# Kernel optimization log

Hardware: AMD Instinct MI355X
Metric: run time of the kernel (lower is better)

## Reference

```python
import jax, jax.numpy as jnp
import numpy as np
from jax import lax


def conv3d(x, w, b):
    # x: [B,C,H,W,D], w: [O,I,kh,kw,kd], SAME padding (matches padding=k//2 for odd k)
    out = lax.conv_general_dilated(
        x, w, window_strides=(1, 1, 1), padding='SAME',
        dimension_numbers=('NCDHW', 'OIDHW', 'NCDHW'))
    return out + b[None, :, None, None, None]


def setup_inputs() -> dict:
    key = jax.random.key(0)
    ks = jax.random.split(key, 9)
    B, C, H, W, D = 2, 64, 16, 16, 16
    P = 64  # pab_channels
    s = 0.05
    return {
        'x': jax.random.normal(ks[0], (B, C, H, W, D), jnp.float32),
        'top_w': jax.random.normal(ks[1], (P, C, 1, 1, 1), jnp.float32) * s,
        'top_b': jax.random.normal(ks[2], (P,), jnp.float32) * s,
        'center_w': jax.random.normal(ks[3], (P, C, 1, 1, 1), jnp.float32) * s,
        'center_b': jax.random.normal(ks[4], (P,), jnp.float32) * s,
        'bottom_w': jax.random.normal(ks[5], (C, C, 3, 3, 3), jnp.float32) * s,
        'bottom_b': jax.random.normal(ks[6], (C,), jnp.float32) * s,
        'out_w': jax.random.normal(ks[7], (C, C, 3, 3, 3), jnp.float32) * s,
        'out_b': jax.random.normal(ks[8], (C,), jnp.float32) * s,
    }


def reference(x, top_w, top_b, center_w, center_b, bottom_w, bottom_b, out_w, out_b):
    B, C, H, W, D = x.shape
    N = H * W * D
    x_top = conv3d(x, top_w, top_b).reshape(B, -1, N)            # [B,P,N]
    x_center = conv3d(x, center_w, center_b).reshape(B, -1, N)   # [B,P,N]
    x_bottom = conv3d(x, bottom_w, bottom_b).reshape(B, C, N)    # [B,C,N]
    # sp_map[b,n,m] = sum_p center[b,p,n] * top[b,p,m]
    sp = jnp.einsum('bpn,bpm->bnm', x_center, x_top)             # [B,N,N]
    # GLOBAL softmax over the entire flattened NxN map per batch element
    sp = jax.nn.softmax(sp.reshape(B, N * N), axis=1).reshape(B, N, N)
    sp = jnp.einsum('bnm,bcm->bnc', sp, x_bottom)                # [B,N,C]
    # faithful to torch: plain reshape [B,N,C] -> [B,C,H,W,D] (no transpose)
    sp = sp.reshape(B, C, H, W, D)
    return conv3d(x + sp, out_w, out_b)
```

## Files before the change

### kernel.cpp

```cpp
#include <hip/hip_runtime.h>


typedef __attribute__((ext_vector_type(8))) short bf16x8;
typedef __attribute__((ext_vector_type(4))) short short4v;
typedef __attribute__((ext_vector_type(4))) float f32x4;

#define DEVI static __device__ __forceinline__

DEVI f32x4 MFMA16(bf16x8 a, bf16x8 b, f32x4 c) {
  return __builtin_amdgcn_mfma_f32_16x16x32_bf16(a, b, c, 0, 0, 0);
}
DEVI f32x4 zero4() { return (f32x4){0.f, 0.f, 0.f, 0.f}; }

DEVI unsigned short f2bf(float f) {
  unsigned u = __float_as_uint(f);
  return (unsigned short)((u + 0x7fffu + ((u >> 16) & 1u)) >> 16);
}
DEVI float bf2f(unsigned short u) { return __uint_as_float((unsigned)u << 16); }
DEVI float fexp2(float x) { return __builtin_amdgcn_exp2f(x); }

DEVI void gll16(const unsigned short* g, unsigned short* l) {
  __builtin_amdgcn_global_load_lds(
      (const __attribute__((address_space(1))) void*)g,
      (__attribute__((address_space(3))) void*)l, 16, 0, 0);
}

__global__ void k_prep(const float* __restrict__ tw, const float* __restrict__ cw,
                       const float* __restrict__ bw, const float* __restrict__ ow,
                       const float* __restrict__ x,
                       unsigned short* __restrict__ wkTopF, unsigned short* __restrict__ wkCenF,
                       unsigned short* __restrict__ wkBotF, unsigned short* __restrict__ wkOutF,
                       unsigned short* __restrict__ xT, unsigned short* __restrict__ zbuf) {
  __shared__ float tile[64][65];
  int bx = blockIdx.x;
  int tid = threadIdx.x;
  if (bx == 0 && tid < 64) zbuf[tid] = 0;
  if (bx < 432) {
    int t = bx * 256 + tid;
    if (t < 4096) {
      int co = t >> 6, ci = t & 63;
      int cog = co >> 4, col = co & 15, kc = ci >> 5, kg = (ci & 31) >> 3, e = ci & 7;
      int dst = (((cog * 2 + kc) * 64) + col + 16 * kg) * 8 + e;
      wkTopF[dst] = f2bf(tw[t]);
      wkCenF[dst] = f2bf(cw[t]);
    }
    int k = t % 27;
    int ci = (t / 27) & 63;
    int co = t / (27 * 64);
    int cog = co >> 4, col = co & 15, kc = ci >> 5, kg = (ci & 31) >> 3, e = ci & 7;
    int dst = ((((cog * 27 + k) * 2 + kc) * 64) + col + 16 * kg) * 8 + e;
    wkBotF[dst] = f2bf(bw[t]);
    wkOutF[dst] = f2bf(ow[t]);
    return;
  }
  int bx2 = bx - 432;
  int b = bx2 >> 6;
  int n0 = (bx2 & 63) << 6;
  {
    int nl = tid & 63, cq = tid >> 6;
    const float* xb = x + (size_t)b * 262144;
#pragma unroll
    for (int j = 0; j < 16; j++) {
      int c = cq * 16 + j;
      tile[c][nl] = xb[(size_t)c * 4096 + n0 + nl];
    }
  }
  __syncthreads();
  {
    int n = tid >> 2, c0 = (tid & 3) << 4;
    bf16x8 o0, o1;
#pragma unroll
    for (int j = 0; j < 8; j++) {
      o0[j] = (short)f2bf(tile[c0 + j][n]);
      o1[j] = (short)f2bf(tile[c0 + 8 + j][n]);
    }
    unsigned short* dst = xT + ((size_t)(b * 4096 + n0 + n)) * 64 + c0;
    *(bf16x8*)(dst) = o0;
    *(bf16x8*)(dst + 8) = o1;
  }
}

template <int OMODE>
DEVI void conv3_body(int bx, int t,
                     const unsigned short* __restrict__ wkF,
                     const unsigned short* __restrict__ xTb,
                     const float* __restrict__ bias,
                     const unsigned short* __restrict__ zbuf,
                     float* __restrict__ outF, unsigned short* __restrict__ outH,
                     unsigned short* hl) {
  int ch = bx & 1, wp = (bx >> 1) & 7, h = (bx >> 4) & 15, b = bx >> 8;
  int lane = t & 63, w = t >> 6;
  int col = lane & 15, kg = lane >> 4;
  const unsigned short* xb = xTb + (size_t)b * 262144;
  int row8 = lane >> 3, blk = lane & 7;
#pragma unroll
  for (int q = 0; q < 6; q++) {
    int vi0 = w * 48 + q * 8;
    int vi = vi0 + row8;
    int dhv = vi >> 6, wv = (vi >> 4) & 3, dv = vi & 15;
    int hh = h + dhv - 1, ww = wp * 2 + wv - 1;
    bool val = ((unsigned)hh < 16u) & ((unsigned)ww < 16u);
    int sw = blk ^ (vi & 7);
    const unsigned short* src =
        val ? (xb + ((size_t)((hh * 256 + ww * 16 + dv)) << 6) + sw * 8) : (zbuf + blk * 8);
    gll16(src, hl + vi0 * 64);
  }
  __syncthreads();
  int wi = w >> 1;
  int cg = ch * 2 + (w & 1);
  const char* hlb = (const char*)hl;
  f32x4 acc0 = zero4(), acc1 = zero4();
#pragma unroll
  for (int k = 0; k < 27; k++) {
    const int dh = k / 9;
    const int dw = (k / 3) % 3;
    const int dz = k % 3 - 1;
    int dsum = col + dz;
    bool vd = (unsigned)dsum < 16u;
    int dcl = vd ? dsum : col;
    int sv = dh * 64 + (wi + dw) * 16 + dcl;
    const unsigned short* wfk = wkF + (((size_t)(cg * 27 + k)) << 10) + lane * 8;
#pragma unroll
    for (int kc = 0; kc < 2; kc++) {
      bf16x8 av = *(const bf16x8*)(wfk + (kc << 9));
      int g = (kc * 4 + kg) ^ (sv & 7);
      bf16x8 bv = *(const bf16x8*)(hlb + sv * 128 + g * 16);
      if (!vd) bv = (bf16x8){0, 0, 0, 0, 0, 0, 0, 0};
      if (kc == 0) acc0 = MFMA16(av, bv, acc0);
      else acc1 = MFMA16(av, bv, acc1);
    }
  }
  int n0c = h * 256 + (wp * 2 + wi) * 16 + col;
#pragma unroll
  for (int r = 0; r < 4; r++) {
    int co = ch * 32 + (w & 1) * 16 + kg * 4 + r;
    float v = acc0[r] + acc1[r] + bias[co];
    if (OMODE == 2)
      outH[(size_t)(b * 64 + co) * 4096 + n0c] = f2bf(v);
    else
      outF[(size_t)(b * 64 + co) * 4096 + n0c] = v;
  }
}

__global__ __launch_bounds__(256, 2) void k_convA(
    const unsigned short* __restrict__ wkTf, const unsigned short* __restrict__ wkCf,
    const unsigned short* __restrict__ wkBf, const unsigned short* __restrict__ xTb,
    const float* __restrict__ tbias, const float* __restrict__ cbias,
    const float* __restrict__ bbias, const unsigned short* __restrict__ zbuf,
    unsigned short* __restrict__ topT, unsigned short* __restrict__ cenT,
    unsigned short* __restrict__ botS) {
  __shared__ __align__(16) unsigned short hl[192 * 64];
  int bx0 = blockIdx.x;
  int t = threadIdx.x;
  if (bx0 >= 512) {
    conv3_body<2>(bx0 - 512, t, wkBf, xTb, bbias, zbuf, nullptr, botS, hl);
    return;
  }
  int lane = t & 63, wid = t >> 6;
  int col = lane & 15, kg = lane >> 4;
  int bx = bx0;
  int b = bx >> 8;
  int rest = bx & 255;
  int nt = rest >> 1, ch = rest & 1;
  int cg = ch * 2 + (wid >> 1);
  int co0 = ch * 32 + (wid >> 1) * 16;
  int n0c = nt * 32 + (wid & 1) * 16 + col;
  const unsigned short* xb = xTb + (size_t)b * 262144;
  f32x4 aT0 = zero4(), aT1 = zero4(), aC0 = zero4(), aC1 = zero4();
#pragma unroll
  for (int kc = 0; kc < 2; kc++) {
    bf16x8 bv = *(const bf16x8*)(xb + (size_t)n0c * 64 + kc * 32 + kg * 8);
    bf16x8 avT = *(const bf16x8*)(wkTf + (((size_t)cg * 2 + kc) * 64 + lane) * 8);
    bf16x8 avC = *(const bf16x8*)(wkCf + (((size_t)cg * 2 + kc) * 64 + lane) * 8);
    if (kc == 0) {
      aT0 = MFMA16(avT, bv, aT0);
      aC0 = MFMA16(avC, bv, aC0);
    } else {
      aT1 = MFMA16(avT, bv, aT1);
      aC1 = MFMA16(avC, bv, aC1);
    }
  }
  const float LOG2E = 1.4426950408889634f;
  short4v sT, sC;
#pragma unroll
  for (int r = 0; r < 4; r++) {
    float bvT = tbias[co0 + kg * 4 + r];
    float bvC = cbias[co0 + kg * 4 + r];
    sT[r] = (short)f2bf(aT0[r] + aT1[r] + bvT);
    sC[r] = (short)f2bf((aC0[r] + aC1[r] + bvC) * LOG2E);
  }
  size_t o = (size_t)(b * 4096 + n0c) * 64 + co0 + kg * 4;
  *(short4v*)(topT + o) = sT;
  *(short4v*)(cenT + o) = sC;
}

__global__ __launch_bounds__(256, 2) void k_convOut(
    const unsigned short* __restrict__ wkOf, const unsigned short* __restrict__ xTb,
    const float* __restrict__ bias, const unsigned short* __restrict__ zbuf,
    float* __restrict__ outF) {
  __shared__ __align__(16) unsigned short hl[192 * 64];
  conv3_body<1>(blockIdx.x, threadIdx.x, wkOf, xTb, bias, zbuf, outF, nullptr, hl);
}

__global__ __launch_bounds__(256, 2) void k_pass2(
    const unsigned short* __restrict__ cenT, const unsigned short* __restrict__ topT,
    const unsigned short* __restrict__ botS,
    unsigned short* __restrict__ part, float* __restrict__ Zpart) {
  __shared__ __align__(16) unsigned short topS[2][4096];
  __shared__ __align__(16) unsigned short botL[2][4096];
  __shared__ __align__(16) unsigned short pT[4][2][1024];
  __shared__ float zred[4];
  int bx = blockIdx.x;
  int b = bx >> 8;
  int ntp = (bx >> 3) & 31;
  int mc = bx & 7;
  int t = threadIdx.x;
  int lane = t & 63, w = t >> 6;
  int col = lane & 15, kg = lane >> 4;
  const unsigned short* cb = cenT + (size_t)b * 262144;
  const unsigned short* tb = topT + (size_t)b * 262144;
  const unsigned short* bb = botS + (size_t)b * 262144;
  int nA = ntp * 128 + w * 16;
  int mcBase = mc * 512;
  int row8 = lane >> 3, blk = lane & 7;
  int sw = blk ^ (row8 & 7);

  bf16x8 aA0 = *(const bf16x8*)(cb + (size_t)(nA + col) * 64 + kg * 8);
  bf16x8 aA1 = *(const bf16x8*)(cb + (size_t)(nA + col) * 64 + 32 + kg * 8);
  bf16x8 aB0 = *(const bf16x8*)(cb + (size_t)(nA + 64 + col) * 64 + kg * 8);
  bf16x8 aB1 = *(const bf16x8*)(cb + (size_t)(nA + 64 + col) * 64 + 32 + kg * 8);

  if (w < 2) {
#pragma unroll
    for (int q = 0; q < 4; q++) {
      int s = w * 4 + q;
      gll16(tb + (size_t)(mcBase + s * 8 + row8) * 64 + sw * 8, &topS[0][s * 512]);
    }
  } else {
#pragma unroll
    for (int q = 0; q < 4; q++) {
      int s = (w - 2) * 4 + q;
      gll16(bb + (size_t)(s * 8 + row8) * 4096 + mcBase + sw * 8, &botL[0][s * 512]);
    }
  }
  __syncthreads();

  f32x4 accOA[4], accOB[4];
#pragma unroll
  for (int ct = 0; ct < 4; ct++) {
    accOA[ct] = zero4();
    accOB[ct] = zero4();
  }
  float zs = 0.f;
  int swc = (col & 7) << 3;
  unsigned short* pw0 = &pT[w][0][0];
  unsigned short* pw1 = &pT[w][1][0];

  for (int j = 0; j < 8; j++) {
    int cur = j & 1;
    if (j < 7) {
      int m0n = mcBase + (j + 1) * 64;
      if (w < 2) {
#pragma unroll
        for (int q = 0; q < 4; q++) {
          int s = w * 4 + q;
          gll16(tb + (size_t)(m0n + s * 8 + row8) * 64 + sw * 8, &topS[cur ^ 1][s * 512]);
        }
      } else {
#pragma unroll
        for (int q = 0; q < 4; q++) {
          int s = (w - 2) * 4 + q;
          gll16(bb + (size_t)(s * 8 + row8) * 4096 + m0n + sw * 8, &botL[cur ^ 1][s * 512]);
        }
      }
    }
    f32x4 sA[4], sB[4];
#pragma unroll
    for (int mt = 0; mt < 4; mt++) {
      bf16x8 b0 = *(const bf16x8*)&topS[cur][(mt * 16 + col) * 64 + ((kg * 8) ^ swc)];
      bf16x8 b1 = *(const bf16x8*)&topS[cur][(mt * 16 + col) * 64 + ((32 + kg * 8) ^ swc)];
      sA[mt] = MFMA16(aA1, b1, MFMA16(aA0, b0, zero4()));
      sB[mt] = MFMA16(aB1, b1, MFMA16(aB0, b0, zero4()));
    }
#pragma unroll
    for (int mt = 0; mt < 4; mt++)
#pragma unroll
      for (int r = 0; r < 4; r++) {
        int nrow = kg * 4 + r;
        int msw = (mt * 16 + col) ^ ((nrow & 7) << 3);
        float eA = fexp2(sA[mt][r]);
        float eB = fexp2(sB[mt][r]);
        zs += eA + eB;
        pw0[nrow * 64 + msw] = f2bf(eA);
        pw1[nrow * 64 + msw] = f2bf(eB);
      }
#pragma unroll
    for (int kc = 0; kc < 2; kc++) {
      bf16x8 paA = *(const bf16x8*)&pw0[col * 64 + ((kc * 32 + kg * 8) ^ swc)];
      bf16x8 paB = *(const bf16x8*)&pw1[col * 64 + ((kc * 32 + kg * 8) ^ swc)];
#pragma unroll
      for (int ct = 0; ct < 4; ct++) {
        bf16x8 bv = *(const bf16x8*)&botL[cur][(ct * 16 + col) * 64 + ((kc * 32 + kg * 8) ^ swc)];
        accOA[ct] = MFMA16(paA, bv, accOA[ct]);
        accOB[ct] = MFMA16(paB, bv, accOB[ct]);
      }
    }
    __syncthreads();
  }
  unsigned short* po = part + (((size_t)(b * 8 + mc) * 4096 + nA) << 6);
#pragma unroll
  for (int ct = 0; ct < 4; ct++)
#pragma unroll
    for (int r = 0; r < 4; r++) {
      po[(kg * 4 + r) * 64 + ct * 16 + col] = f2bf(accOA[ct][r]);
      po[(64 + kg * 4 + r) * 64 + ct * 16 + col] = f2bf(accOB[ct][r]);
    }
#pragma unroll
  for (int off = 32; off; off >>= 1) zs += __shfl_xor(zs, off);
  if (lane == 0) zred[w] = zs;
  __syncthreads();
  if (t == 0) Zpart[b * 256 + ntp * 8 + mc] = zred[0] + zred[1] + zred[2] + zred[3];
}

__global__ void k_xt1(const float* __restrict__ x, const unsigned short* __restrict__ part,
                      const float* __restrict__ Zpart, unsigned short* __restrict__ xT) {
  __shared__ float tile[64][65];
  __shared__ float zr[4];
  int bx = blockIdx.x;
  int b = bx >> 6;
  int n0 = (bx & 63) << 6;
  int t = threadIdx.x;
  float zv = Zpart[b * 256 + t];
#pragma unroll
  for (int off = 32; off; off >>= 1) zv += __shfl_xor(zv, off);
  if ((t & 63) == 0) zr[t >> 6] = zv;
  __syncthreads();
  float invZ = 1.0f / (zr[0] + zr[1] + zr[2] + zr[3]);
  {
    int nl = t & 63, cq = t >> 6;
    const float* xb = x + (size_t)b * 262144;
    int nt6 = n0 >> 6;
#pragma unroll
    for (int j = 0; j < 16; j++) {
      int c = cq * 16 + j;
      float v = xb[(size_t)c * 4096 + n0 + nl];
      float s = 0.f;
#pragma unroll
      for (int mcq = 0; mcq < 8; mcq++)
        s += bf2f(part[(((size_t)(b * 8 + mcq) * 4096) + c * 64 + nt6) * 64 + nl]);
      tile[c][nl] = v + s * invZ;
    }
  }
  __syncthreads();
  {
    int n = t >> 2, c0 = (t & 3) << 4;
    bf16x8 o0, o1;
#pragma unroll
    for (int j = 0; j < 8; j++) {
      o0[j] = (short)f2bf(tile[c0 + j][n]);
      o1[j] = (short)f2bf(tile[c0 + 8 + j][n]);
    }
    unsigned short* dst = xT + ((size_t)(b * 4096 + n0 + n)) * 64 + c0;
    *(bf16x8*)(dst) = o0;
    *(bf16x8*)(dst + 8) = o1;
  }
}

extern "C" void kernel_launch(void* const* d_in, const int* in_sizes, int n_in,
                              void* d_out, int out_size, void* d_ws, size_t ws_size,
                              hipStream_t stream) {
  const float* x = (const float*)d_in[0];
  const float* tw = (const float*)d_in[1];
  const float* tb = (const float*)d_in[2];
  const float* cw = (const float*)d_in[3];
  const float* cbb = (const float*)d_in[4];
  const float* bw = (const float*)d_in[5];
  const float* bb = (const float*)d_in[6];
  const float* ow = (const float*)d_in[7];
  const float* ob = (const float*)d_in[8];
  float* out = (float*)d_out;
  char* ws = (char*)d_ws;

  unsigned short* wkTopF = (unsigned short*)(ws + 0);
  unsigned short* wkCenF = (unsigned short*)(ws + 8192);
  unsigned short* wkBotF = (unsigned short*)(ws + 16384);
  unsigned short* wkOutF = (unsigned short*)(ws + 237568);
  unsigned short* xT = (unsigned short*)(ws + 458752);
  unsigned short* topT = (unsigned short*)(ws + 1507328);
  unsigned short* cenT = (unsigned short*)(ws + 2555904);
  unsigned short* botS = (unsigned short*)(ws + 3604480);
  unsigned short* yT = (unsigned short*)(ws + 4653056);
  unsigned short* part = (unsigned short*)(ws + 5701632);
  float* Zpart = (float*)(ws + 14090240);
  unsigned short* zbuf = (unsigned short*)(ws + 14092288);

  k_prep<<<560, 256, 0, stream>>>(tw, cw, bw, ow, x, wkTopF, wkCenF, wkBotF, wkOutF, xT, zbuf);
  k_convA<<<1024, 256, 0, stream>>>(wkTopF, wkCenF, wkBotF, xT, tb, cbb, bb, zbuf, topT, cenT, botS);
  k_pass2<<<512, 256, 0, stream>>>(cenT, topT, botS, part, Zpart);
  k_xt1<<<128, 256, 0, stream>>>(x, part, Zpart, yT);
  k_convOut<<<512, 256, 0, stream>>>(wkOutF, yT, ob, zbuf, out);
}
```

Measured before the change: 46.70 us.

## Keep softmax probabilities in registers via swapped MFMA operands; vectorize partial reduction

In the attention pass, the score MFMA operands are swapped so each lane's accumulator layout matches the A-operand layout of the following P·V MFMA. The exponentiated scores are then packed straight to bf16 in registers with v_cvt_pk_bf16_f32, which removes the per-wave LDS round-trip for the probability tile. The bottom-feature B operand is now read as two 4-element halves with a matching K permutation. Separately, the partial-sum reduction kernel loads bf16 partials and x in 16-byte vectors instead of scalar loads. The risks are extra LDS read instructions for the split B loads and a subtle dependence on the permuted K ordering being correct.

```diff
diff --git a/kernel.cpp b/kernel.cpp
--- a/kernel.cpp
+++ b/kernel.cpp
@@ -18,6 +18,26 @@
 }
 DEVI float bf2f(unsigned short u) { return __uint_as_float((unsigned)u << 16); }
 DEVI float fexp2(float x) { return __builtin_amdgcn_exp2f(x); }
+
+DEVI unsigned cvtpk(float lo, float hi) {
+  unsigned d;
+  asm("v_cvt_pk_bf16_f32 %0, %1, %2" : "=v"(d) : "v"(lo), "v"(hi));
+  return d;
+}
+DEVI bf16x8 pack8(f32x4 a, f32x4 b) {
+  union { unsigned u[4]; bf16x8 v; } r;
+  r.u[0] = cvtpk(a[0], a[1]);
+  r.u[1] = cvtpk(a[2], a[3]);
+  r.u[2] = cvtpk(b[0], b[1]);
+  r.u[3] = cvtpk(b[2], b[3]);
+  return r.v;
+}
+DEVI bf16x8 cat44(short4v lo, short4v hi) {
+  union { short4v s[2]; bf16x8 v; } c;
+  c.s[0] = lo;
+  c.s[1] = hi;
+  return c.v;
+}
 
 DEVI void gll16(const unsigned short* g, unsigned short* l) {
   __builtin_amdgcn_global_load_lds(
@@ -208,7 +228,6 @@
     unsigned short* __restrict__ part, float* __restrict__ Zpart) {
   __shared__ __align__(16) unsigned short topS[2][4096];
   __shared__ __align__(16) unsigned short botL[2][4096];
-  __shared__ __align__(16) unsigned short pT[4][2][1024];
   __shared__ float zred[4];
   int bx = blockIdx.x;
   int b = bx >> 8;
@@ -253,8 +272,12 @@
   }
   float zs = 0.f;
   int swc = (col & 7) << 3;
-  unsigned short* pw0 = &pT[w][0][0];
-  unsigned short* pw1 = &pT[w][1][0];
+  int bofs[2][2];
+#pragma unroll
+  for (int kc = 0; kc < 2; kc++) {
+    bofs[kc][0] = (((kc * 4 + (kg >> 1)) ^ (col & 7)) << 3) + (kg & 1) * 4;
+    bofs[kc][1] = (((kc * 4 + 2 + (kg >> 1)) ^ (col & 7)) << 3) + (kg & 1) * 4;
+  }
 
   for (int j = 0; j < 8; j++) {
     int cur = j & 1;
@@ -279,28 +302,27 @@
     for (int mt = 0; mt < 4; mt++) {
       bf16x8 b0 = *(const bf16x8*)&topS[cur][(mt * 16 + col) * 64 + ((kg * 8) ^ swc)];
       bf16x8 b1 = *(const bf16x8*)&topS[cur][(mt * 16 + col) * 64 + ((32 + kg * 8) ^ swc)];
-      sA[mt] = MFMA16(aA1, b1, MFMA16(aA0, b0, zero4()));
-      sB[mt] = MFMA16(aB1, b1, MFMA16(aB0, b0, zero4()));
+      sA[mt] = MFMA16(b1, aA1, MFMA16(b0, aA0, zero4()));
+      sB[mt] = MFMA16(b1, aB1, MFMA16(b0, aB0, zero4()));
     }
 #pragma unroll
     for (int mt = 0; mt < 4; mt++)
 #pragma unroll
       for (int r = 0; r < 4; r++) {
-        int nrow = kg * 4 + r;
-        int msw = (mt * 16 + col) ^ ((nrow & 7) << 3);
-        float eA = fexp2(sA[mt][r]);
-        float eB = fexp2(sB[mt][r]);
-        zs += eA + eB;
-        pw0[nrow * 64 + msw] = f2bf(eA);
-        pw1[nrow * 64 + msw] = f2bf(eB);
+        sA[mt][r] = fexp2(sA[mt][r]);
+        sB[mt][r] = fexp2(sB[mt][r]);
+        zs += sA[mt][r] + sB[mt][r];
       }
 #pragma unroll
     for (int kc = 0; kc < 2; kc++) {
-      bf16x8 paA = *(const bf16x8*)&pw0[col * 64 + ((kc * 32 + kg * 8) ^ swc)];
-      bf16x8 paB = *(const bf16x8*)&pw1[col * 64 + ((kc * 32 + kg * 8) ^ swc)];
+      bf16x8 paA = pack8(sA[2 * kc], sA[2 * kc + 1]);
+      bf16x8 paB = pack8(sB[2 * kc], sB[2 * kc + 1]);
 #pragma unroll
       for (int ct = 0; ct < 4; ct++) {
-        bf16x8 bv = *(const bf16x8*)&botL[cur][(ct * 16 + col) * 64 + ((kc * 32 + kg * 8) ^ swc)];
+        const unsigned short* brow = &botL[cur][(ct * 16 + col) * 64];
+        short4v lo = *(const short4v*)(brow + bofs[kc][0]);
+        short4v hi = *(const short4v*)(brow + bofs[kc][1]);
+        bf16x8 bv = cat44(lo, hi);
         accOA[ct] = MFMA16(paA, bv, accOA[ct]);
         accOB[ct] = MFMA16(paB, bv, accOB[ct]);
       }
@@ -337,18 +359,29 @@
   __syncthreads();
   float invZ = 1.0f / (zr[0] + zr[1] + zr[2] + zr[3]);
   {
-    int nl = t & 63, cq = t >> 6;
-    const float* xb = x + (size_t)b * 262144;
+    int c = t >> 2, nl16 = (t & 3) << 4;
     int nt6 = n0 >> 6;
-#pragma unroll
-    for (int j = 0; j < 16; j++) {
-      int c = cq * 16 + j;
-      float v = xb[(size_t)c * 4096 + n0 + nl];
-      float s = 0.f;
-#pragma unroll
-      for (int mcq = 0; mcq < 8; mcq++)
-        s += bf2f(part[(((size_t)(b * 8 + mcq) * 4096) + c * 64 + nt6) * 64 + nl]);
-      tile[c][nl] = v + s * invZ;
+    float acc[16];
+#pragma unroll
+    for (int k = 0; k < 16; k++) acc[k] = 0.f;
+#pragma unroll
+    for (int mcq = 0; mcq < 8; mcq++) {
+      const unsigned short* pp =
+          part + (((size_t)(b * 8 + mcq) * 4096) + c * 64 + nt6) * 64 + nl16;
+      bf16x8 v0 = *(const bf16x8*)pp;
+      bf16x8 v1 = *(const bf16x8*)(pp + 8);
+#pragma unroll
+      for (int k = 0; k < 8; k++) {
+        acc[k] += bf2f((unsigned short)v0[k]);
+        acc[8 + k] += bf2f((unsigned short)v1[k]);
+      }
+    }
+    const float* xb = x + (size_t)b * 262144 + (size_t)c * 4096 + n0 + nl16;
+#pragma unroll
+    for (int q = 0; q < 4; q++) {
+      f32x4 xv = *(const f32x4*)(xb + q * 4);
+#pragma unroll
+      for (int k = 0; k < 4; k++) tile[c][nl16 + q * 4 + k] = xv[k] + acc[q * 4 + k] * invZ;
     }
   }
   __syncthreads();
```

Measured after the change: 48.13 us. +3.1%, slower.
